# Kernel tuning notes

Measured on AMD Instinct MI355X. Metric: run time of the kernel, lower is better.

Reference implementation:

```python
import jax, jax.numpy as jnp
import numpy as np

C_ENC = 64
H_FEAT = 96
W_FEAT = 96
B = 2
Q = 32768
HID = 256
IN_DIM = C_ENC * 9 + 2 + 2  # 580
EPS_SHIFT = 1e-6


def _unfold3x3(feat):
    # F.unfold(feat, 3, padding=1).view(B, C*9, H, W)
    Bf, C, H, W = feat.shape
    p = jnp.pad(feat, ((0, 0), (0, 0), (1, 1), (1, 1)))
    shifts = [p[:, :, ki:ki + H, kj:kj + W] for ki in range(3) for kj in range(3)]
    return jnp.stack(shifts, axis=2).reshape(Bf, C * 9, H, W)


def _nearest_idx(g, size):
    # torch grid_sample nearest, align_corners=False: unnormalize then nearbyint
    ix = ((g + 1.0) * size - 1.0) * 0.5
    return jnp.clip(jnp.round(ix).astype(jnp.int32), 0, size - 1)


def _mlp(x, W0, b0, W1, b1, W2, b2, W3, b3, W4, b4):
    h = jax.nn.relu(x @ W0 + b0)
    h = jax.nn.relu(h @ W1 + b1)
    h = jax.nn.relu(h @ W2 + b2)
    h = jax.nn.relu(h @ W3 + b3)
    return h @ W4 + b4


def setup_inputs() -> dict:
    key = jax.random.key(0)
    ks = jax.random.split(key, 8)
    feat = jax.random.normal(ks[0], (B, C_ENC, H_FEAT, W_FEAT), jnp.float32)
    coord = jax.random.uniform(ks[1], (B, Q, 2), jnp.float32, -1.0, 1.0)
    # cell size for a ~181x181 HR grid: 2/181
    cell = jnp.full((B, Q, 2), 2.0 / 181.0, jnp.float32)
    s0 = 1.0 / np.sqrt(IN_DIM)
    sh = 1.0 / np.sqrt(HID)
    W0 = jax.random.normal(ks[2], (IN_DIM, HID), jnp.float32) * s0
    W1 = jax.random.normal(ks[3], (HID, HID), jnp.float32) * sh
    W2 = jax.random.normal(ks[4], (HID, HID), jnp.float32) * sh
    W3 = jax.random.normal(ks[5], (HID, HID), jnp.float32) * sh
    W4 = jax.random.normal(ks[6], (HID, 1), jnp.float32) * sh
    z = lambda n: jnp.zeros((n,), jnp.float32)
    return {"feat": feat, "coord": coord, "cell": cell,
            "W0": W0, "b0": z(HID), "W1": W1, "b1": z(HID),
            "W2": W2, "b2": z(HID), "W3": W3, "b3": z(HID),
            "W4": W4, "b4": z(1)}


def reference(feat, coord, cell, W0, b0, W1, b1, W2, b2, W3, b3, W4, b4):
    Bf, C, H, W = feat.shape
    feat_u = _unfold3x3(feat)                     # (B, C*9, H, W)
    feat_flat = feat_u.reshape(Bf, C * 9, H * W)  # (B, C9, HW)
    rx = 1.0 / H  # 2 / H / 2
    ry = 1.0 / W
    lo, hi = -1.0 + 1e-6, 1.0 - 1e-6
    rel_cell = cell * jnp.array([H, W], jnp.float32)  # (B,Q,2)

    preds, areas = [], []
    for vx in (-1.0, 1.0):
        for vy in (-1.0, 1.0):
            c0 = jnp.clip(coord[..., 0] + vx * rx + EPS_SHIFT, lo, hi)
            c1 = jnp.clip(coord[..., 1] + vy * ry + EPS_SHIFT, lo, hi)
            iy = _nearest_idx(c0, H)   # (B,Q) index into H dim
            ix = _nearest_idx(c1, W)
            lin = iy * W + ix
            q_feat = jnp.take_along_axis(feat_flat, lin[:, None, :], axis=2)
            q_feat = q_feat.transpose(0, 2, 1)  # (B,Q,C9)
            # pixel-center coords (= gathered make_coord grid)
            qc0 = (iy.astype(jnp.float32) + 0.5) * (2.0 / H) - 1.0
            qc1 = (ix.astype(jnp.float32) + 0.5) * (2.0 / W) - 1.0
            rel0 = (coord[..., 0] - qc0) * H
            rel1 = (coord[..., 1] - qc1) * W
            inp = jnp.concatenate(
                [q_feat, rel0[..., None], rel1[..., None], rel_cell], axis=-1)
            pred = _mlp(inp.reshape(Bf * inp.shape[1], -1),
                        W0, b0, W1, b1, W2, b2, W3, b3, W4, b4)
            preds.append(pred.reshape(Bf, -1, 1))
            areas.append(jnp.abs(rel0 * rel1) + 1e-9)

    tot_area = areas[0] + areas[1] + areas[2] + areas[3]
    # local-ensemble diagonal swap of areas
    areas = [areas[3], areas[2], areas[1], areas[0]]
    ret = jnp.zeros_like(preds[0])
    for pred, area in zip(preds, areas):
        ret = ret + pred * (area / tot_area)[..., None]
    return ret
```

## Files before the change

kernel.cpp:

```cpp
#include <hip/hip_runtime.h>
#include <hip/hip_bf16.h>

typedef __attribute__((ext_vector_type(8))) short bf16x8;
typedef __attribute__((ext_vector_type(4))) float f32x4;

__device__ inline ushort f2bf(float f) {
    union { float f; unsigned u; } x; x.f = f;
    unsigned u = x.u;
    u += 0x7fffu + ((u >> 16) & 1u);
    return (ushort)(u >> 16);
}

__global__ void prep_feat_k(const float* __restrict__ feat, ushort* __restrict__ featT) {
    int idx = blockIdx.x * 256 + threadIdx.x;
    if (idx >= 2 * 98 * 98 * 64) return;
    int c = idx & 63;
    int rest = idx >> 6;
    int x = rest % 98; rest /= 98;
    int y = rest % 98;
    int b = rest / 98;
    ushort v = 0;
    if (x >= 1 && x <= 96 && y >= 1 && y <= 96)
        v = f2bf(feat[((b * 64 + c) * 96 + (y - 1)) * 96 + (x - 1)]);
    featT[idx] = v;
}

__global__ void prep_w_k(const float* __restrict__ W, ushort* __restrict__ Wp,
                         int NT, int NKT, int Nstride, int mode) {
    int idx = blockIdx.x * 256 + threadIdx.x;
    if (idx >= NT * NKT * 64) return;
    int lane = idx & 63;
    int kt = (idx >> 6) % NKT;
    int nt = idx / (64 * NKT);
    int n = nt * 16 + (lane & 15);
    int kbase = kt * 32 + (lane >> 4) * 8;
    ushort o[8];
    #pragma unroll
    for (int i = 0; i < 8; ++i) {
        int k = kbase + i;
        float v = 0.0f;
        if (mode == 0) {
            if (k < 576) { int tap = k >> 6, c = k & 63; v = W[(c * 9 + tap) * Nstride + n]; }
            else if (k < 580) v = W[k * Nstride + n];
        } else if (mode == 1) {
            v = W[k * Nstride + n];
        } else {
            v = (n == 0) ? W[k] : 0.0f;
        }
        o[i] = f2bf(v);
    }
    *reinterpret_cast<uint4*>(Wp + (size_t)idx * 8) = *reinterpret_cast<const uint4*>(o);
}

__global__ __launch_bounds__(256, 3) void liif_main(
    const float* __restrict__ coord, const float* __restrict__ cell,
    const ushort* __restrict__ featT,
    const ushort* __restrict__ W0p, const ushort* __restrict__ W1p,
    const ushort* __restrict__ W2p, const ushort* __restrict__ W3p,
    const ushort* __restrict__ W4p,
    const float* __restrict__ b0, const float* __restrict__ b1,
    const float* __restrict__ b2, const float* __restrict__ b3,
    const float* __restrict__ b4, float* __restrict__ out)
{
    __shared__ ushort buf[4 * 8 * 64 * 8];
    __shared__ float pred_lds[64];
    __shared__ float area_lds[64];

    const int t = threadIdx.x;
    const int lane = t & 63;
    const int w = t >> 6;
    const int g = lane >> 4;
    const int l15 = lane & 15;
    const int swl = lane ^ (((lane >> 3) & 3) << 2);

    const int r = t >> 2, sub = t & 3;
    const int qi = r >> 2, s = r & 3;
    const int gq = blockIdx.x * 16 + qi;
    const int bidx = gq >> 15;
    int iy, ix;
    float rel0, rel1, rc0, rc1;
    {
        const float vx = (s & 2) ? 1.0f : -1.0f;
        const float vy = (s & 1) ? 1.0f : -1.0f;
        const float rxf = (float)(1.0 / 96.0);
        const float lo = (float)(-1.0 + 1e-6);
        const float hi = (float)(1.0 - 1e-6);
        float c0 = coord[gq * 2 + 0], c1 = coord[gq * 2 + 1];
        float cl0 = cell[gq * 2 + 0], cl1 = cell[gq * 2 + 1];
        float sc0 = fminf(fmaxf(__fadd_rn(__fadd_rn(c0, vx * rxf), 1e-6f), lo), hi);
        float sc1 = fminf(fmaxf(__fadd_rn(__fadd_rn(c1, vy * rxf), 1e-6f), lo), hi);
        float fy = __fmul_rn(__fadd_rn(__fmul_rn(__fadd_rn(sc0, 1.0f), 96.0f), -1.0f), 0.5f);
        float fx = __fmul_rn(__fadd_rn(__fmul_rn(__fadd_rn(sc1, 1.0f), 96.0f), -1.0f), 0.5f);
        iy = (int)rintf(fy); iy = iy < 0 ? 0 : (iy > 95 ? 95 : iy);
        ix = (int)rintf(fx); ix = ix < 0 ? 0 : (ix > 95 ? 95 : ix);
        float qc0 = (iy + 0.5f) * (float)(2.0 / 96.0) - 1.0f;
        float qc1 = (ix + 0.5f) * (float)(2.0 / 96.0) - 1.0f;
        rel0 = (c0 - qc0) * 96.0f;
        rel1 = (c1 - qc1) * 96.0f;
        rc0 = cl0 * 96.0f; rc1 = cl1 * 96.0f;
        if (sub == 0) area_lds[r] = fabsf(rel0 * rel1) + 1e-9f;
    }
    const int g_rt = r >> 4;
    const int g_slot = (r & 15) + (sub << 4);
    const int g_sw = g_slot ^ (((g_slot >> 3) & 3) << 2);
    const ushort* p0 = featT + (size_t)bidx * 98 * 98 * 64 + (iy * 98 + ix) * 64 + sub * 8;

    ushort* sp[4];
    #pragma unroll
    for (int ct = 0; ct < 4; ++ct) {
        int col = (w * 4 + ct) * 16 + l15;
        int ktc = col >> 5;
        int chk = (col & 31) >> 3;
        int slot0 = (chk << 4) + g * 4;
        int sw0 = slot0 ^ (((slot0 >> 3) & 3) << 2);
        sp[ct] = buf + (ktc * 64 + sw0) * 8 + (col & 7);
    }

    f32x4 acc[4][4];

    auto store_acts = [&]() {
        #pragma unroll
        for (int ct = 0; ct < 4; ++ct)
            #pragma unroll
            for (int rt = 0; rt < 4; ++rt) {
                float v0 = fmaxf(acc[rt][ct][0], 0.0f);
                float v1 = fmaxf(acc[rt][ct][1], 0.0f);
                float v2 = fmaxf(acc[rt][ct][2], 0.0f);
                float v3 = fmaxf(acc[rt][ct][3], 0.0f);
                uint p01, p23;
                asm("v_cvt_pk_bf16_f32 %0, %1, %2" : "=v"(p01) : "v"(v0), "v"(v1));
                asm("v_cvt_pk_bf16_f32 %0, %1, %2" : "=v"(p23) : "v"(v2), "v"(v3));
                ushort* sptr = sp[ct] + rt * 4096;
                sptr[0]  = (ushort)p01;
                sptr[8]  = (ushort)(p01 >> 16);
                sptr[16] = (ushort)p23;
                sptr[24] = (ushort)(p23 >> 16);
            }
    };

    auto init_acc = [&](const float* bias) {
        #pragma unroll
        for (int ct = 0; ct < 4; ++ct) {
            float bv = bias[(w * 4 + ct) * 16 + l15];
            #pragma unroll
            for (int rt = 0; rt < 4; ++rt) {
                acc[rt][ct][0] = bv; acc[rt][ct][1] = bv;
                acc[rt][ct][2] = bv; acc[rt][ct][3] = bv;
            }
        }
    };

    auto l1_mfma = [&](int kt, int line) {
        bf16x8 bfr[4];
        #pragma unroll
        for (int ct = 0; ct < 4; ++ct)
            bfr[ct] = *reinterpret_cast<const bf16x8*>(W0p + (((size_t)(w * 4 + ct) * 19 + kt) * 64 + lane) * 8);
        #pragma unroll
        for (int rt = 0; rt < 4; ++rt) {
            bf16x8 a = *reinterpret_cast<const bf16x8*>(buf + ((rt * 8 + line) * 64 + swl) * 8);
            #pragma unroll
            for (int ct = 0; ct < 4; ++ct)
                acc[rt][ct] = __builtin_amdgcn_mfma_f32_16x16x32_bf16(a, bfr[ct], acc[rt][ct], 0, 0, 0);
        }
    };

    auto lx_mfma = [&](const ushort* Wp, int kt) {
        bf16x8 bfr[4];
        #pragma unroll
        for (int ct = 0; ct < 4; ++ct)
            bfr[ct] = *reinterpret_cast<const bf16x8*>(Wp + (((size_t)(w * 4 + ct) * 8 + kt) * 64 + lane) * 8);
        #pragma unroll
        for (int rt = 0; rt < 4; ++rt) {
            bf16x8 a = *reinterpret_cast<const bf16x8*>(buf + ((rt * 8 + kt) * 64 + swl) * 8);
            #pragma unroll
            for (int ct = 0; ct < 4; ++ct)
                acc[rt][ct] = __builtin_amdgcn_mfma_f32_16x16x32_bf16(a, bfr[ct], acc[rt][ct], 0, 0, 0);
        }
    };

#define G1(KT, LINE) do {                                                        \
        constexpr int tap_ = (KT) >> 1;                                          \
        constexpr int coff_ = ((tap_ / 3) * 98 + (tap_ % 3)) * 64 + ((KT) & 1) * 32; \
        *reinterpret_cast<uint4*>(&buf[((g_rt * 8 + (LINE)) * 64 + g_sw) * 8]) = \
            *reinterpret_cast<const uint4*>(p0 + coff_);                         \
    } while (0)

    init_acc(b0);
    G1(0, 0); G1(1, 1); G1(2, 2); G1(3, 3); G1(4, 4); G1(5, 5); G1(6, 6); G1(7, 7);
    __syncthreads();
    __builtin_amdgcn_s_setprio(1);
    #pragma unroll 1
    for (int i = 0; i < 8; ++i) l1_mfma(i, i);
    __builtin_amdgcn_s_setprio(0);
    __syncthreads();
    G1(8, 0); G1(9, 1); G1(10, 2); G1(11, 3); G1(12, 4); G1(13, 5); G1(14, 6); G1(15, 7);
    __syncthreads();
    __builtin_amdgcn_s_setprio(1);
    #pragma unroll 1
    for (int i = 0; i < 8; ++i) l1_mfma(8 + i, i);
    __builtin_amdgcn_s_setprio(0);
    __syncthreads();
    G1(16, 0); G1(17, 1);
    {
        ushort ex[8] = {0, 0, 0, 0, 0, 0, 0, 0};
        if (sub == 0) {
            ex[0] = f2bf(rel0); ex[1] = f2bf(rel1);
            ex[2] = f2bf(rc0);  ex[3] = f2bf(rc1);
        }
        *reinterpret_cast<uint4*>(&buf[((g_rt * 8 + 2) * 64 + g_sw) * 8]) =
            *reinterpret_cast<const uint4*>(ex);
    }
    __syncthreads();
    __builtin_amdgcn_s_setprio(1);
    l1_mfma(16, 0); l1_mfma(17, 1); l1_mfma(18, 2);
    __builtin_amdgcn_s_setprio(0);
    __syncthreads();

    #pragma unroll 1
    for (int layer = 0; layer < 3; ++layer) {
        store_acts();
        const ushort* Wp = (layer == 0) ? W1p : (layer == 1) ? W2p : W3p;
        const float* bias = (layer == 0) ? b1 : (layer == 1) ? b2 : b3;
        init_acc(bias);
        __builtin_amdgcn_s_setprio(1);
        lx_mfma(Wp, 2 * w);
        lx_mfma(Wp, 2 * w + 1);
        __builtin_amdgcn_s_setprio(0);
        __syncthreads();
        __builtin_amdgcn_s_setprio(1);
        #pragma unroll 1
        for (int i = 2; i < 8; ++i) lx_mfma(Wp, (2 * w + i) & 7);
        __builtin_amdgcn_s_setprio(0);
        __syncthreads();
    }
    store_acts();
    __syncthreads();

    {
        float b4v = b4[0];
        f32x4 a5;
        a5[0] = b4v; a5[1] = b4v; a5[2] = b4v; a5[3] = b4v;
        #pragma unroll
        for (int kt = 0; kt < 8; ++kt) {
            bf16x8 bb = *reinterpret_cast<const bf16x8*>(W4p + ((size_t)kt * 64 + lane) * 8);
            bf16x8 aa = *reinterpret_cast<const bf16x8*>(buf + ((w * 8 + kt) * 64 + swl) * 8);
            a5 = __builtin_amdgcn_mfma_f32_16x16x32_bf16(aa, bb, a5, 0, 0, 0);
        }
        if (l15 == 0) {
            #pragma unroll
            for (int j = 0; j < 4; ++j)
                pred_lds[w * 16 + (g << 2) + j] = a5[j];
        }
    }
    __syncthreads();

    if (t < 16) {
        int oq = blockIdx.x * 16 + t;
        float p0v = pred_lds[t * 4 + 0], p1v = pred_lds[t * 4 + 1];
        float p2v = pred_lds[t * 4 + 2], p3v = pred_lds[t * 4 + 3];
        float a0 = area_lds[t * 4 + 0], a1 = area_lds[t * 4 + 1];
        float a2 = area_lds[t * 4 + 2], a3 = area_lds[t * 4 + 3];
        float tot = a0 + a1 + a2 + a3;
        out[oq] = (p0v * a3 + p1v * a2 + p2v * a1 + p3v * a0) / tot;
    }
#undef G1
}

extern "C" void kernel_launch(void* const* d_in, const int* in_sizes, int n_in,
                              void* d_out, int out_size, void* d_ws, size_t ws_size,
                              hipStream_t stream) {
    const float* feat  = (const float*)d_in[0];
    const float* coord = (const float*)d_in[1];
    const float* cell  = (const float*)d_in[2];
    const float* W0 = (const float*)d_in[3];
    const float* b0 = (const float*)d_in[4];
    const float* W1 = (const float*)d_in[5];
    const float* b1 = (const float*)d_in[6];
    const float* W2 = (const float*)d_in[7];
    const float* b2 = (const float*)d_in[8];
    const float* W3 = (const float*)d_in[9];
    const float* b3 = (const float*)d_in[10];
    const float* W4 = (const float*)d_in[11];
    const float* b4 = (const float*)d_in[12];
    float* out = (float*)d_out;

    ushort* featT = (ushort*)d_ws;
    ushort* W0p = featT + 1229312;
    ushort* W1p = W0p + 155648;
    ushort* W2p = W1p + 65536;
    ushort* W3p = W2p + 65536;
    ushort* W4p = W3p + 65536;

    prep_feat_k<<<4802, 256, 0, stream>>>(feat, featT);
    prep_w_k<<<76, 256, 0, stream>>>(W0, W0p, 16, 19, 256, 0);
    prep_w_k<<<32, 256, 0, stream>>>(W1, W1p, 16, 8, 256, 1);
    prep_w_k<<<32, 256, 0, stream>>>(W2, W2p, 16, 8, 256, 1);
    prep_w_k<<<32, 256, 0, stream>>>(W3, W3p, 16, 8, 256, 1);
    prep_w_k<<<2, 256, 0, stream>>>(W4, W4p, 1, 8, 1, 2);
    liif_main<<<4096, 256, 0, stream>>>(coord, cell, featT, W0p, W1p, W2p, W3p, W4p,
                                        b0, b1, b2, b3, b4, out);
}
```

Before: 206.8 us.

## Double-buffer weight fragment loads, retune LDS swizzle, raise occupancy target

Weight B-fragments for the next k-tile are now loaded into registers while the current tile's MFMAs run, so global/L2 load latency overlaps with matrix work. The LDS XOR swizzle is changed to a new pattern, with a matching lane-dependent permutation of the packed bf16 values on the activation store path, aimed at reducing bank conflicts. Launch bounds go from 3 to 4 blocks per CU. The extra prefetch registers combined with the tighter register budget from the higher occupancy target could cause spills.

```diff
diff --git a/kernel.cpp b/kernel.cpp
--- a/kernel.cpp
+++ b/kernel.cpp
@@ -52,7 +52,9 @@
     *reinterpret_cast<uint4*>(Wp + (size_t)idx * 8) = *reinterpret_cast<const uint4*>(o);
 }
 
-__global__ __launch_bounds__(256, 3) void liif_main(
+__device__ __forceinline__ int SW(int slot) { return slot ^ ((slot >> 2) & 7); }
+
+__global__ __launch_bounds__(256, 4) void liif_main(
     const float* __restrict__ coord, const float* __restrict__ cell,
     const ushort* __restrict__ featT,
     const ushort* __restrict__ W0p, const ushort* __restrict__ W1p,
@@ -71,7 +73,7 @@
     const int w = t >> 6;
     const int g = lane >> 4;
     const int l15 = lane & 15;
-    const int swl = lane ^ (((lane >> 3) & 3) << 2);
+    const int swl = SW(lane);
 
     const int r = t >> 2, sub = t & 3;
     const int qi = r >> 2, s = r & 3;
@@ -101,8 +103,7 @@
         if (sub == 0) area_lds[r] = fabsf(rel0 * rel1) + 1e-9f;
     }
     const int g_rt = r >> 4;
-    const int g_slot = (r & 15) + (sub << 4);
-    const int g_sw = g_slot ^ (((g_slot >> 3) & 3) << 2);
+    const int g_sw = SW((r & 15) + (sub << 4));
     const ushort* p0 = featT + (size_t)bidx * 98 * 98 * 64 + (iy * 98 + ix) * 64 + sub * 8;
 
     ushort* sp[4];
@@ -112,8 +113,9 @@
         int ktc = col >> 5;
         int chk = (col & 31) >> 3;
         int slot0 = (chk << 4) + g * 4;
-        int sw0 = slot0 ^ (((slot0 >> 3) & 3) << 2);
-        sp[ct] = buf + (ktc * 64 + sw0) * 8 + (col & 7);
+        int m = (slot0 >> 2) & 7;
+        int swb = (slot0 ^ m) & ~3;
+        sp[ct] = buf + (ktc * 64 + swb) * 8 + (col & 7);
     }
 
     f32x4 acc[4][4];
@@ -130,11 +132,17 @@
                 uint p01, p23;
                 asm("v_cvt_pk_bf16_f32 %0, %1, %2" : "=v"(p01) : "v"(v0), "v"(v1));
                 asm("v_cvt_pk_bf16_f32 %0, %1, %2" : "=v"(p23) : "v"(v2), "v"(v3));
+                uint t01 = (g & 2) ? p23 : p01;
+                uint t23 = (g & 2) ? p01 : p23;
+                uint r01 = (t01 >> 16) | (t01 << 16);
+                uint r23 = (t23 >> 16) | (t23 << 16);
+                t01 = (g & 1) ? r01 : t01;
+                t23 = (g & 1) ? r23 : t23;
                 ushort* sptr = sp[ct] + rt * 4096;
-                sptr[0]  = (ushort)p01;
-                sptr[8]  = (ushort)(p01 >> 16);
-                sptr[16] = (ushort)p23;
-                sptr[24] = (ushort)(p23 >> 16);
+                sptr[0]  = (ushort)t01;
+                sptr[8]  = (ushort)(t01 >> 16);
+                sptr[16] = (ushort)t23;
+                sptr[24] = (ushort)(t23 >> 16);
             }
     };
 
@@ -150,34 +158,25 @@
         }
     };
 
-    auto l1_mfma = [&](int kt, int line) {
-        bf16x8 bfr[4];
-        #pragma unroll
-        for (int ct = 0; ct < 4; ++ct)
-            bfr[ct] = *reinterpret_cast<const bf16x8*>(W0p + (((size_t)(w * 4 + ct) * 19 + kt) * 64 + lane) * 8);
-        #pragma unroll
-        for (int rt = 0; rt < 4; ++rt) {
-            bf16x8 a = *reinterpret_cast<const bf16x8*>(buf + ((rt * 8 + line) * 64 + swl) * 8);
-            #pragma unroll
-            for (int ct = 0; ct < 4; ++ct)
-                acc[rt][ct] = __builtin_amdgcn_mfma_f32_16x16x32_bf16(a, bfr[ct], acc[rt][ct], 0, 0, 0);
-        }
-    };
-
-    auto lx_mfma = [&](const ushort* Wp, int kt) {
-        bf16x8 bfr[4];
-        #pragma unroll
-        for (int ct = 0; ct < 4; ++ct)
-            bfr[ct] = *reinterpret_cast<const bf16x8*>(Wp + (((size_t)(w * 4 + ct) * 8 + kt) * 64 + lane) * 8);
-        #pragma unroll
-        for (int rt = 0; rt < 4; ++rt) {
-            bf16x8 a = *reinterpret_cast<const bf16x8*>(buf + ((rt * 8 + kt) * 64 + swl) * 8);
-            #pragma unroll
-            for (int ct = 0; ct < 4; ++ct)
-                acc[rt][ct] = __builtin_amdgcn_mfma_f32_16x16x32_bf16(a, bfr[ct], acc[rt][ct], 0, 0, 0);
-        }
-    };
-
+#define LOADW0(DST, KT) do { _Pragma("unroll")                                   \
+        for (int ct_ = 0; ct_ < 4; ++ct_)                                        \
+            DST[ct_] = *reinterpret_cast<const bf16x8*>(                         \
+                W0p + (((size_t)(w * 4 + ct_) * 19 + (KT)) * 64 + lane) * 8);    \
+    } while (0)
+#define LOADWX(DST, WP, KT) do { _Pragma("unroll")                               \
+        for (int ct_ = 0; ct_ < 4; ++ct_)                                        \
+            DST[ct_] = *reinterpret_cast<const bf16x8*>(                         \
+                (WP) + (((size_t)(w * 4 + ct_) * 8 + (KT)) * 64 + lane) * 8);    \
+    } while (0)
+#define MFMA_LINE(BFR, LINE) do { _Pragma("unroll")                              \
+        for (int rt_ = 0; rt_ < 4; ++rt_) {                                      \
+            bf16x8 a_ = *reinterpret_cast<const bf16x8*>(                        \
+                buf + ((rt_ * 8 + (LINE)) * 64 + swl) * 8);                      \
+            _Pragma("unroll")                                                    \
+            for (int ct_ = 0; ct_ < 4; ++ct_)                                    \
+                acc[rt_][ct_] = __builtin_amdgcn_mfma_f32_16x16x32_bf16(         \
+                    a_, BFR[ct_], acc[rt_][ct_], 0, 0, 0);                       \
+        } } while (0)
 #define G1(KT, LINE) do {                                                        \
         constexpr int tap_ = (KT) >> 1;                                          \
         constexpr int coff_ = ((tap_ / 3) * 98 + (tap_ % 3)) * 64 + ((KT) & 1) * 32; \
@@ -186,18 +185,31 @@
     } while (0)
 
     init_acc(b0);
+    bf16x8 cur[4], nxt[4];
     G1(0, 0); G1(1, 1); G1(2, 2); G1(3, 3); G1(4, 4); G1(5, 5); G1(6, 6); G1(7, 7);
+    LOADW0(cur, 0);
     __syncthreads();
     __builtin_amdgcn_s_setprio(1);
     #pragma unroll 1
-    for (int i = 0; i < 8; ++i) l1_mfma(i, i);
+    for (int i = 0; i < 8; ++i) {
+        if (i < 7) LOADW0(nxt, i + 1);
+        MFMA_LINE(cur, i);
+        #pragma unroll
+        for (int c_ = 0; c_ < 4; ++c_) cur[c_] = nxt[c_];
+    }
     __builtin_amdgcn_s_setprio(0);
     __syncthreads();
     G1(8, 0); G1(9, 1); G1(10, 2); G1(11, 3); G1(12, 4); G1(13, 5); G1(14, 6); G1(15, 7);
+    LOADW0(cur, 8);
     __syncthreads();
     __builtin_amdgcn_s_setprio(1);
     #pragma unroll 1
-    for (int i = 0; i < 8; ++i) l1_mfma(8 + i, i);
+    for (int i = 0; i < 8; ++i) {
+        if (i < 7) LOADW0(nxt, 9 + i);
+        MFMA_LINE(cur, i);
+        #pragma unroll
+        for (int c_ = 0; c_ < 4; ++c_) cur[c_] = nxt[c_];
+    }
     __builtin_amdgcn_s_setprio(0);
     __syncthreads();
     G1(16, 0); G1(17, 1);
@@ -210,9 +222,18 @@
         *reinterpret_cast<uint4*>(&buf[((g_rt * 8 + 2) * 64 + g_sw) * 8]) =
             *reinterpret_cast<const uint4*>(ex);
     }
+    LOADW0(cur, 16);
     __syncthreads();
     __builtin_amdgcn_s_setprio(1);
-    l1_mfma(16, 0); l1_mfma(17, 1); l1_mfma(18, 2);
+    LOADW0(nxt, 17);
+    MFMA_LINE(cur, 0);
+    #pragma unroll
+    for (int c_ = 0; c_ < 4; ++c_) cur[c_] = nxt[c_];
+    LOADW0(nxt, 18);
+    MFMA_LINE(cur, 1);
+    #pragma unroll
+    for (int c_ = 0; c_ < 4; ++c_) cur[c_] = nxt[c_];
+    MFMA_LINE(cur, 2);
     __builtin_amdgcn_s_setprio(0);
     __syncthreads();
 
@@ -222,14 +243,24 @@
         const ushort* Wp = (layer == 0) ? W1p : (layer == 1) ? W2p : W3p;
         const float* bias = (layer == 0) ? b1 : (layer == 1) ? b2 : b3;
         init_acc(bias);
+        LOADWX(cur, Wp, 2 * w);
         __builtin_amdgcn_s_setprio(1);
-        lx_mfma(Wp, 2 * w);
-        lx_mfma(Wp, 2 * w + 1);
+        LOADWX(nxt, Wp, 2 * w + 1);
+        MFMA_LINE(cur, 2 * w);
+        #pragma unroll
+        for (int c_ = 0; c_ < 4; ++c_) cur[c_] = nxt[c_];
+        LOADWX(nxt, Wp, (2 * w + 2) & 7);
+        MFMA_LINE(cur, 2 * w + 1);
         __builtin_amdgcn_s_setprio(0);
         __syncthreads();
         __builtin_amdgcn_s_setprio(1);
         #pragma unroll 1
-        for (int i = 2; i < 8; ++i) lx_mfma(Wp, (2 * w + i) & 7);
+        for (int i = 2; i < 8; ++i) {
+            #pragma unroll
+            for (int c_ = 0; c_ < 4; ++c_) cur[c_] = nxt[c_];
+            if (i < 7) LOADWX(nxt, Wp, (2 * w + i + 1) & 7);
+            MFMA_LINE(cur, (2 * w + i) & 7);
+        }
         __builtin_amdgcn_s_setprio(0);
         __syncthreads();
     }
@@ -264,6 +295,9 @@
         out[oq] = (p0v * a3 + p1v * a2 + p2v * a1 + p3v * a0) / tot;
     }
 #undef G1
+#undef LOADW0
+#undef LOADWX
+#undef MFMA_LINE
 }
 
 extern "C" void kernel_launch(void* const* d_in, const int* in_sizes, int n_in,
```

Measured after the change: 210.9 us. About the same (+2.0%).
